# Kernel optimization log

Hardware: AMD Instinct MI355X
Metric: run time of the kernel (lower is better)

## Reference

```python
import jax, jax.numpy as jnp
import numpy as np

CHANNELS = 25
BN_EPS = 1e-5


def _diff(x):
    # x: [B,H,W]; zero-pad by 1 on H and W, then shifted slices (same as torch diff())
    xp = jnp.pad(x, ((0, 0), (1, 1), (1, 1)))
    p_x = (xp[:, 2:, 1:-1] - xp[:, :-2, 1:-1]) / 2
    p_y = (xp[:, 1:-1, 2:] - xp[:, 1:-1, :-2]) / 2
    pp_x = xp[:, 2:, 1:-1] + xp[:, :-2, 1:-1] - 2 * x
    pp_y = xp[:, 1:-1, 2:] + xp[:, 1:-1, :-2] - 2 * x
    pp_xy = xp[:, 2:, 2:] + xp[:, :-2, :-2] - xp[:, 2:, 1:-1] - xp[:, 1:-1, 2:]
    return p_x, p_y, pp_x, pp_y, pp_xy


def _batchnorm(x, gamma, beta):
    # x: [B,C,H,W]; training-mode BN with batch statistics (biased variance)
    mean = jnp.mean(x, axis=(0, 2, 3), keepdims=True)
    var = jnp.mean((x - mean) ** 2, axis=(0, 2, 3), keepdims=True)
    xhat = (x - mean) * jax.lax.rsqrt(var + BN_EPS)
    return xhat * gamma[None, :, None, None] + beta[None, :, None, None]


def setup_inputs() -> dict:
    key = jax.random.key(0)
    ks = jax.random.split(key, 5)
    B, H, W = 32, 512, 512
    x = jax.random.normal(ks[0], (B, H, W), dtype=jnp.float32)
    # 1x1 conv weights stored as [out_ch, in_ch]
    w1 = jax.random.normal(ks[1], (CHANNELS, 6), dtype=jnp.float32) * (1.0 / np.sqrt(6.0))
    b1 = jnp.zeros((CHANNELS,), dtype=jnp.float32)
    g1 = jnp.ones((CHANNELS,), dtype=jnp.float32)
    beta1 = jnp.zeros((CHANNELS,), dtype=jnp.float32)
    w2 = jax.random.normal(ks[2], (1, CHANNELS), dtype=jnp.float32) * (1.0 / np.sqrt(CHANNELS))
    b2 = jnp.zeros((1,), dtype=jnp.float32)
    g2 = jnp.ones((1,), dtype=jnp.float32)
    beta2 = jnp.zeros((1,), dtype=jnp.float32)
    return {"x": x, "w1": w1, "b1": b1, "g1": g1, "beta1": beta1,
            "w2": w2, "b2": b2, "g2": g2, "beta2": beta2}


def reference(x, w1, b1, g1, beta1, w2, b2, g2, beta2):
    p_x, p_y, pp_x, pp_y, pp_xy = _diff(x)
    xx = jnp.stack([x, p_x, p_y, pp_x, pp_y, pp_xy], axis=1)  # [B,6,H,W]
    # 1x1 conv == per-pixel channel matmul
    h = jnp.einsum('bchw,oc->bohw', xx, w1) + b1[None, :, None, None]
    h = jax.nn.relu(_batchnorm(h, g1, beta1))  # [B,25,H,W]
    o = jnp.einsum('bchw,oc->bohw', h, w2) + b2[None, :, None, None]
    o = jax.nn.relu(_batchnorm(o, g2, beta2))[:, 0, :, :]  # [B,H,W]
    return o + x
```

## Files before the change

kernel.cpp:

```cpp
#include <hip/hip_runtime.h>
#include <hip/hip_fp16.h>

typedef float f4 __attribute__((ext_vector_type(4)));
typedef float f2 __attribute__((ext_vector_type(2)));
typedef _Float16 f16x8 __attribute__((ext_vector_type(8)));
typedef float f32x16 __attribute__((ext_vector_type(16)));

#define NPIX (32*512*512)
#define BN_EPS 1e-5f


struct Rows { f4 C, N, S; float wv, ev, nwv, sev; };

__device__ __forceinline__ Rows loadrows(const float* __restrict__ x,
                                         const float* zbuf, int p) {
    Rows r;
    int rem = p & (512*512 - 1);
    int i = rem >> 9, jj = rem & 511;
    const float* xc = x + p;
    const float* xn = (i > 0)   ? xc - 512 : zbuf;
    const float* xs = (i < 511) ? xc + 512 : zbuf;
    r.C = *(const f4*)xc;
    r.N = *(const f4*)xn;
    r.S = *(const f4*)xs;
    bool hw = (jj > 0), he = (jj < 508);
    float wv  = xc[hw ? -1 : 0];
    float ev  = xc[he ?  4 : 3];
    float nwv = xn[hw ? -1 : 0];
    float sev = xs[he ?  4 : 3];
    r.wv  = hw ? wv  : 0.f;
    r.ev  = he ? ev  : 0.f;
    r.nwv = hw ? nwv : 0.f;
    r.sev = he ? sev : 0.f;
    return r;
}

__device__ __forceinline__ void mkstencil(const Rows& r, f4* s) {
    f4 E   = {r.C.y, r.C.z, r.C.w, r.ev};
    f4 W   = {r.wv,  r.C.x, r.C.y, r.C.z};
    f4 Ssh = {r.S.y, r.S.z, r.S.w, r.sev};
    f4 Nsh = {r.nwv, r.N.x, r.N.y, r.N.z};
    s[0] = r.C;
    s[1] = (r.S - r.N) * 0.5f;
    s[2] = (E - W) * 0.5f;
    s[3] = r.S + r.N - 2.f*r.C;
    s[4] = E + W - 2.f*r.C;
    s[5] = Ssh + Nsh - r.S - E;
}

__global__ __launch_bounds__(256) void k_moments(const float* __restrict__ x,
                                                 const float* __restrict__ ws,
                                                 float* __restrict__ outp) {
    const float* zbuf = ws + 496;
    int t = threadIdx.x;
    int g0 = blockIdx.x * 1024 + t;
    f2 acc[27];
    #pragma unroll
    for (int i = 0; i < 27; ++i) acc[i] = (f2){0.f, 0.f};

    #pragma unroll
    for (int q = 0; q < 4; ++q) {
        Rows r = loadrows(x, zbuf, (g0 + 256*q) * 4);
        f4 s[6];
        mkstencil(r, s);
        #pragma unroll
        for (int a = 0; a < 6; ++a) {
            f2 alo = s[a].xy, ahi = s[a].zw;
            asm("v_pk_add_f32 %0, %1, %0" : "+v"(acc[a]) : "v"(alo));
            asm("v_pk_add_f32 %0, %1, %0" : "+v"(acc[a]) : "v"(ahi));
            #pragma unroll
            for (int b = a; b < 6; ++b) {
                int idx = 6 + a*(11-a)/2 + b;
                f2 blo = s[b].xy, bhi = s[b].zw;
                asm("v_pk_fma_f32 %0, %1, %2, %0" : "+v"(acc[idx]) : "v"(alo), "v"(blo));
                asm("v_pk_fma_f32 %0, %1, %2, %0" : "+v"(acc[idx]) : "v"(ahi), "v"(bhi));
            }
        }
    }
    __shared__ float red[27][4];
    int wave = t >> 6, lane = t & 63;
    #pragma unroll
    for (int i = 0; i < 27; ++i) {
        float v = acc[i].x + acc[i].y;
        for (int off = 32; off; off >>= 1) v += __shfl_xor(v, off);
        if (lane == 0) red[i][wave] = v;
    }
    __syncthreads();
    if (t < 27)
        outp[t*2048 + blockIdx.x] = red[t][0] + red[t][1] + red[t][2] + red[t][3];
}

__global__ __launch_bounds__(256) void k_red(const float* __restrict__ outp,
                                             float* __restrict__ ws) {
    int b = blockIdx.x;
    int t = threadIdx.x;
    float v = 0.f;
    #pragma unroll
    for (int k = 0; k < 8; ++k) v += outp[b*2048 + t + 256*k];
    for (int off = 32; off; off >>= 1) v += __shfl_xor(v, off);
    __shared__ float red[4];
    int wave = t >> 6, lane = t & 63;
    if (lane == 0) red[wave] = v;
    __syncthreads();
    if (t == 0) ws[b] = red[0] + red[1] + red[2] + red[3];
}

__global__ void k_stats1(const float* w1, const float* b1, const float* g1,
                         const float* beta1, const float* w2, float* ws) {
    __shared__ float sm[32][8];
    int c = threadIdx.x;
    if (c < 32) {
        #pragma unroll
        for (int k = 0; k < 8; ++k) sm[c][k] = 0.f;
        ws[64 + c] = (c < 25) ? w2[c] : 0.f;
    }
    __syncthreads();
    if (c < 25) {
        const float invN = 1.f / (float)NPIX;
        float m1[6], wr[6];
        #pragma unroll
        for (int i = 0; i < 6; ++i) m1[i] = ws[i] * invN;
        #pragma unroll
        for (int i = 0; i < 6; ++i) wr[i] = w1[c*6 + i];
        float bc = b1[c];
        float mean = bc;
        #pragma unroll
        for (int i = 0; i < 6; ++i) mean = fmaf(wr[i], m1[i], mean);
        float e2 = bc * bc;
        #pragma unroll
        for (int i = 0; i < 6; ++i) e2 = fmaf(2.f*bc*wr[i], m1[i], e2);
        #pragma unroll
        for (int i = 0; i < 6; ++i)
            #pragma unroll
            for (int j = 0; j < 6; ++j) {
                int a = i < j ? i : j, b = i < j ? j : i;
                float m2 = ws[6 + a*(11-a)/2 + b] * invN;
                e2 = fmaf(wr[i]*wr[j], m2, e2);
            }
        float var = e2 - mean*mean;
        float a1 = g1[c] * rsqrtf(var + BN_EPS);
        #pragma unroll
        for (int i = 0; i < 6; ++i) sm[c][i] = a1 * wr[i];
        sm[c][6] = fmaf(a1, bc - mean, beta1[c]);
    }
    __syncthreads();
    int ch = c & 31, h = c >> 5;
    float aC=0.f, aN=0.f, aS=0.f, aE=0.f, aW=0.f, aNW=0.f, aSE=0.f, ab=0.f;
    if (h == 0) {
        float w0 = sm[ch][0], w1v = sm[ch][1], w2v = sm[ch][2];
        float w3 = sm[ch][3], w4v = sm[ch][4], w5 = sm[ch][5], be = sm[ch][6];
        aC  = w0 - 2.f*w3 - 2.f*w4v;
        aN  = -0.5f*w1v + w3;
        aS  =  0.5f*w1v + w3 - w5;
        aE  =  0.5f*w2v + w4v - w5;
        aW  = -0.5f*w2v + w4v;
        aNW = w5;
        aSE = w5;
        ab  = be;
    }
    __half2 p0 = __floats2half2_rn(aC,  aN);
    __half2 p1 = __floats2half2_rn(aS,  aE);
    __half2 p2 = __floats2half2_rn(aW,  aNW);
    __half2 p3 = __floats2half2_rn(aSE, ab);
    unsigned u0, u1, u2, u3;
    __builtin_memcpy(&u0, &p0, 4);
    __builtin_memcpy(&u1, &p1, 4);
    __builtin_memcpy(&u2, &p2, 4);
    __builtin_memcpy(&u3, &p3, 4);
    uint4 fr = {u0, u1, u2, u3};
    ((uint4*)(ws + 96))[c] = fr;
}

__global__ __launch_bounds__(256) void k_main(const float* __restrict__ x,
                                              const float* __restrict__ ws,
                                              const float* __restrict__ b2,
                                              float* __restrict__ stats,
                                              float* __restrict__ opre) {
    int t = threadIdx.x;
    int l = t & 63, wv = t >> 6;
    int lane31 = l & 31, h = l >> 5;
    const float* zb = ws + 1024;

    f16x8 afr;
    {
        uint4 u = ((const uint4*)(ws + 96))[l];
        union { uint4 u; f16x8 v; } cv; cv.u = u; afr = cv.v;
    }
    float w2v[16];
    #pragma unroll
    for (int r = 0; r < 16; ++r) {
        int creg = (r & 3) + 8 * (r >> 2);
        w2v[r] = ws[64 + creg + 4*h];
    }
    f32x16 zacc;
    #pragma unroll
    for (int r = 0; r < 16; ++r) zacc[r] = 0.f;
    float b2v = b2[0];
    float S1 = 0.f, S2 = 0.f;

    int wave_id = blockIdx.x * 4 + wv;
    #pragma unroll 1
    for (int rr = 0; rr < 2; ++rr) {
        int row = wave_id * 2 + rr;
        int i = row & 511;
        const float* xc = x + row * 512 + lane31;
        const float* xn = (i > 0)   ? xc - 512 : zb + lane31;
        const float* xs = (i < 511) ? xc + 512 : zb + lane31;
        float* op = opre + row * 512 + lane31;

        #pragma unroll
        for (int jt = 0; jt < 16; ++jt) {
            const int o4 = jt * 32;
            int offm1 = o4 - 1, offp1 = o4 + 1;
            if (jt == 0  && lane31 == 0)  offm1 = o4;
            if (jt == 15 && lane31 == 31) offp1 = o4;

            float C  = xc[o4];
            float W_ = xc[offm1];
            float E  = xc[offp1];
            float N  = xn[o4];
            float NW = xn[offm1];
            float S_ = xs[o4];
            float SE = xs[offp1];
            if (jt == 0)  { bool ok = (lane31 != 0);  W_ = ok ? W_ : 0.f; NW = ok ? NW : 0.f; }
            if (jt == 15) { bool ok = (lane31 != 31); E  = ok ? E  : 0.f; SE = ok ? SE : 0.f; }

            __half2 p0 = __floats2half2_rn(C,  N);
            __half2 p1 = __floats2half2_rn(S_, E);
            __half2 p2 = __floats2half2_rn(W_, NW);
            __half2 p3 = __floats2half2_rn(SE, 1.f);
            unsigned u0, u1, u2, u3;
            __builtin_memcpy(&u0, &p0, 4);
            __builtin_memcpy(&u1, &p1, 4);
            __builtin_memcpy(&u2, &p2, 4);
            __builtin_memcpy(&u3, &p3, 4);
            union { uint4 u; f16x8 v; } bv;
            bv.u = (uint4){u0, u1, u2, u3};

            f32x16 acc = __builtin_amdgcn_mfma_f32_32x32x16_f16(afr, bv.v, zacc, 0, 0, 0);

            float o = 0.f;
            #pragma unroll
            for (int r = 0; r < 16; ++r)
                o = fmaf(fmaxf(acc[r], 0.f), w2v[r], o);
            o += __shfl_xor(o, 32);
            o += b2v;
            S1 += o;
            S2 = fmaf(o, o, S2);
            if (l < 32) op[o4] = o;
        }
    }

    for (int off = 32; off; off >>= 1) { S1 += __shfl_xor(S1, off); S2 += __shfl_xor(S2, off); }
    __shared__ float red[2][4];
    if (l == 0) { red[0][wv] = S1; red[1][wv] = S2; }
    __syncthreads();
    if (t == 0) stats[2048 + blockIdx.x] = 0.5f*(red[0][0]+red[0][1]+red[0][2]+red[0][3]);
    if (t == 1) stats[4096 + blockIdx.x] = 0.5f*(red[1][0]+red[1][1]+red[1][2]+red[1][3]);
}

__global__ __launch_bounds__(256) void k_redS(float* __restrict__ ws) {
    int t = threadIdx.x;
    float s1 = 0.f, s2 = 0.f;
    #pragma unroll
    for (int k = 0; k < 8; ++k) {
        s1 += ws[2048 + t + 256*k];
        s2 += ws[4096 + t + 256*k];
    }
    for (int off = 32; off; off >>= 1) { s1 += __shfl_xor(s1, off); s2 += __shfl_xor(s2, off); }
    __shared__ float red[2][4];
    int wave = t >> 6, lane = t & 63;
    if (lane == 0) { red[0][wave] = s1; red[1][wave] = s2; }
    __syncthreads();
    if (t == 0) ws[27] = red[0][0] + red[0][1] + red[0][2] + red[0][3];
    if (t == 1) ws[28] = red[1][0] + red[1][1] + red[1][2] + red[1][3];
}

__global__ __launch_bounds__(256) void k_final(const float* __restrict__ x,
                                               const float* __restrict__ ws,
                                               const float* __restrict__ g2,
                                               const float* __restrict__ beta2,
                                               float* __restrict__ out) {
    const float invN = 1.f / (float)NPIX;
    float mean = ws[27] * invN;
    float var  = ws[28] * invN - mean*mean;
    float a2 = g2[0] * rsqrtf(var + BN_EPS);
    float c2 = fmaf(-mean, a2, beta2[0]);

    int idx = blockIdx.x * 256 + threadIdx.x;
    f4 o  = ((const f4*)out)[idx];
    f4 xv = ((const f4*)x)[idx];
    f4 r;
    r.x = fmaxf(fmaf(a2, o.x, c2), 0.f) + xv.x;
    r.y = fmaxf(fmaf(a2, o.y, c2), 0.f) + xv.y;
    r.z = fmaxf(fmaf(a2, o.z, c2), 0.f) + xv.z;
    r.w = fmaxf(fmaf(a2, o.w, c2), 0.f) + xv.w;
    ((f4*)out)[idx] = r;
}

extern "C" void kernel_launch(void* const* d_in, const int* in_sizes, int n_in,
                              void* d_out, int out_size, void* d_ws, size_t ws_size,
                              hipStream_t stream) {
    const float* x     = (const float*)d_in[0];
    const float* w1    = (const float*)d_in[1];
    const float* b1    = (const float*)d_in[2];
    const float* g1    = (const float*)d_in[3];
    const float* beta1 = (const float*)d_in[4];
    const float* w2    = (const float*)d_in[5];
    const float* b2    = (const float*)d_in[6];
    const float* g2    = (const float*)d_in[7];
    const float* beta2 = (const float*)d_in[8];
    float* out = (float*)d_out;
    float* ws  = (float*)d_ws;

    hipMemsetAsync(ws, 0, 8192, stream);
    k_moments<<<2048, 256, 0, stream>>>(x, ws, out);
    k_red    <<<27, 256, 0, stream>>>(out, ws);
    k_stats1 <<<1, 64, 0, stream>>>(w1, b1, g1, beta1, w2, ws);
    k_main   <<<2048, 256, 0, stream>>>(x, ws, b2, ws, out);
    k_redS   <<<1, 256, 0, stream>>>(ws);
    k_final  <<<8192, 256, 0, stream>>>(x, ws, g2, beta2, out);
}
```

Before: 100.2 us.

## Compute stencil second moments with MFMA Gram matrix and pack epilogue FMAs

The moments kernel now builds the six stencil features per pixel, stores them as fp16 in LDS along with a constant-one row, and accumulates the 7x7 Gram matrix with 32x32x16 MFMA instructions. This replaces the per-thread packed FMA outer products. It also changes the mapping to one wave per two rows with scalar loads. Separately, the main kernel's ReLU and w2 dot product are switched to packed v_pk_fma_f32 with paired weights. The trade-off is that fp16 moments lose precision, and there is extra LDS traffic and wave barriers per 64 pixels.

New measurement: 102.1 us. About the same (+1.9%).

```diff
diff --git a/kernel.cpp b/kernel.cpp
--- a/kernel.cpp
+++ b/kernel.cpp
@@ -10,84 +10,97 @@
 #define BN_EPS 1e-5f
 
 
-struct Rows { f4 C, N, S; float wv, ev, nwv, sev; };
-
-__device__ __forceinline__ Rows loadrows(const float* __restrict__ x,
-                                         const float* zbuf, int p) {
-    Rows r;
-    int rem = p & (512*512 - 1);
-    int i = rem >> 9, jj = rem & 511;
-    const float* xc = x + p;
-    const float* xn = (i > 0)   ? xc - 512 : zbuf;
-    const float* xs = (i < 511) ? xc + 512 : zbuf;
-    r.C = *(const f4*)xc;
-    r.N = *(const f4*)xn;
-    r.S = *(const f4*)xs;
-    bool hw = (jj > 0), he = (jj < 508);
-    float wv  = xc[hw ? -1 : 0];
-    float ev  = xc[he ?  4 : 3];
-    float nwv = xn[hw ? -1 : 0];
-    float sev = xs[he ?  4 : 3];
-    r.wv  = hw ? wv  : 0.f;
-    r.ev  = he ? ev  : 0.f;
-    r.nwv = hw ? nwv : 0.f;
-    r.sev = he ? sev : 0.f;
-    return r;
-}
-
-__device__ __forceinline__ void mkstencil(const Rows& r, f4* s) {
-    f4 E   = {r.C.y, r.C.z, r.C.w, r.ev};
-    f4 W   = {r.wv,  r.C.x, r.C.y, r.C.z};
-    f4 Ssh = {r.S.y, r.S.z, r.S.w, r.sev};
-    f4 Nsh = {r.nwv, r.N.x, r.N.y, r.N.z};
-    s[0] = r.C;
-    s[1] = (r.S - r.N) * 0.5f;
-    s[2] = (E - W) * 0.5f;
-    s[3] = r.S + r.N - 2.f*r.C;
-    s[4] = E + W - 2.f*r.C;
-    s[5] = Ssh + Nsh - r.S - E;
-}
-
 __global__ __launch_bounds__(256) void k_moments(const float* __restrict__ x,
                                                  const float* __restrict__ ws,
                                                  float* __restrict__ outp) {
-    const float* zbuf = ws + 496;
+    __shared__ ushort sl[4][8][64];
+    __shared__ float mom[4][7][7];
     int t = threadIdx.x;
-    int g0 = blockIdx.x * 1024 + t;
-    f2 acc[27];
-    #pragma unroll
-    for (int i = 0; i < 27; ++i) acc[i] = (f2){0.f, 0.f};
-
-    #pragma unroll
-    for (int q = 0; q < 4; ++q) {
-        Rows r = loadrows(x, zbuf, (g0 + 256*q) * 4);
-        f4 s[6];
-        mkstencil(r, s);
-        #pragma unroll
-        for (int a = 0; a < 6; ++a) {
-            f2 alo = s[a].xy, ahi = s[a].zw;
-            asm("v_pk_add_f32 %0, %1, %0" : "+v"(acc[a]) : "v"(alo));
-            asm("v_pk_add_f32 %0, %1, %0" : "+v"(acc[a]) : "v"(ahi));
-            #pragma unroll
-            for (int b = a; b < 6; ++b) {
-                int idx = 6 + a*(11-a)/2 + b;
-                f2 blo = s[b].xy, bhi = s[b].zw;
-                asm("v_pk_fma_f32 %0, %1, %2, %0" : "+v"(acc[idx]) : "v"(alo), "v"(blo));
-                asm("v_pk_fma_f32 %0, %1, %2, %0" : "+v"(acc[idx]) : "v"(ahi), "v"(bhi));
-            }
+    int l = t & 63, wv = t >> 6;
+    int h = l >> 5;
+    const float* zb = ws + 1024;
+
+    sl[wv][6][l] = (ushort)0x3C00;
+    sl[wv][7][l] = (ushort)0;
+
+    f32x16 accA, accB;
+    #pragma unroll
+    for (int r = 0; r < 16; ++r) { accA[r] = 0.f; accB[r] = 0.f; }
+
+    int arow = ((l & 31) < 7) ? (l & 31) : 7;
+    const ushort* rdp = &sl[wv][arow][8*h];
+
+    int wave_id = blockIdx.x * 4 + wv;
+    #pragma unroll 1
+    for (int rr = 0; rr < 2; ++rr) {
+        int row = wave_id * 2 + rr;
+        int i = row & 511;
+        const float* xr = x + row * 512;
+        const float* xn = (i > 0)   ? xr - 512 : zb;
+        const float* xs = (i < 511) ? xr + 512 : zb;
+        #pragma unroll 1
+        for (int it = 0; it < 8; ++it) {
+            int col = it * 64 + l;
+            bool okw = (col > 0), oke = (col < 511);
+            int cm = okw ? col - 1 : 0;
+            int cp = oke ? col + 1 : 511;
+            float C  = xr[col], N = xn[col], S_ = xs[col];
+            float W_ = xr[cm],  E = xr[cp];
+            float NW = xn[cm],  SE = xs[cp];
+            W_ = okw ? W_ : 0.f; NW = okw ? NW : 0.f;
+            E  = oke ? E  : 0.f; SE = oke ? SE : 0.f;
+
+            float s0 = C;
+            float s1 = (S_ - N) * 0.5f;
+            float s2 = (E - W_) * 0.5f;
+            float s3 = S_ + N - 2.f*C;
+            float s4 = E + W_ - 2.f*C;
+            float s5 = SE + NW - S_ - E;
+
+            __half h0 = __float2half(s0), h1 = __float2half(s1);
+            __half h2 = __float2half(s2), h3 = __float2half(s3);
+            __half h4 = __float2half(s4), h5 = __float2half(s5);
+            sl[wv][0][l] = *(ushort*)&h0;
+            sl[wv][1][l] = *(ushort*)&h1;
+            sl[wv][2][l] = *(ushort*)&h2;
+            sl[wv][3][l] = *(ushort*)&h3;
+            sl[wv][4][l] = *(ushort*)&h4;
+            sl[wv][5][l] = *(ushort*)&h5;
+            __builtin_amdgcn_wave_barrier();
+
+            union { uint4 u; f16x8 v; } f0, f1, f2_, f3;
+            f0.u  = *(const uint4*)(rdp);
+            f1.u  = *(const uint4*)(rdp + 16);
+            f2_.u = *(const uint4*)(rdp + 32);
+            f3.u  = *(const uint4*)(rdp + 48);
+            accA = __builtin_amdgcn_mfma_f32_32x32x16_f16(f0.v,  f0.v,  accA, 0, 0, 0);
+            accB = __builtin_amdgcn_mfma_f32_32x32x16_f16(f1.v,  f1.v,  accB, 0, 0, 0);
+            accA = __builtin_amdgcn_mfma_f32_32x32x16_f16(f2_.v, f2_.v, accA, 0, 0, 0);
+            accB = __builtin_amdgcn_mfma_f32_32x32x16_f16(f3.v,  f3.v,  accB, 0, 0, 0);
+            __builtin_amdgcn_wave_barrier();
         }
     }
-    __shared__ float red[27][4];
-    int wave = t >> 6, lane = t & 63;
-    #pragma unroll
-    for (int i = 0; i < 27; ++i) {
-        float v = acc[i].x + acc[i].y;
-        for (int off = 32; off; off >>= 1) v += __shfl_xor(v, off);
-        if (lane == 0) red[i][wave] = v;
-    }
-    __syncthreads();
-    if (t < 27)
-        outp[t*2048 + blockIdx.x] = red[t][0] + red[t][1] + red[t][2] + red[t][3];
+
+    if ((l & 31) < 7) {
+        int j = l & 31;
+        #pragma unroll
+        for (int r = 0; r < 4; ++r) {
+            int irow = r + 4*h;
+            if (irow < 7) mom[wv][irow][j] = accA[r] + accB[r];
+        }
+    }
+    __syncthreads();
+    if (t < 27) {
+        int a, b;
+        if (t < 6) { a = t; b = 6; }
+        else {
+            int rem = t - 6; a = 0;
+            while (rem >= 6 - a) { rem -= 6 - a; ++a; }
+            b = a + rem;
+        }
+        float v = mom[0][a][b] + mom[1][a][b] + mom[2][a][b] + mom[3][a][b];
+        outp[t*2048 + blockIdx.x] = v;
+    }
 }
 
 __global__ __launch_bounds__(256) void k_red(const float* __restrict__ outp,
@@ -186,11 +199,11 @@
         uint4 u = ((const uint4*)(ws + 96))[l];
         union { uint4 u; f16x8 v; } cv; cv.u = u; afr = cv.v;
     }
-    float w2v[16];
-    #pragma unroll
-    for (int r = 0; r < 16; ++r) {
-        int creg = (r & 3) + 8 * (r >> 2);
-        w2v[r] = ws[64 + creg + 4*h];
+    f2 w2p[8];
+    #pragma unroll
+    for (int r2 = 0; r2 < 8; ++r2) {
+        int creg = ((2*r2) & 3) + 8 * ((2*r2) >> 2) + 4*h;
+        w2p[r2] = *(const f2*)(ws + 64 + creg);
     }
     f32x16 zacc;
     #pragma unroll
@@ -239,10 +252,15 @@
 
             f32x16 acc = __builtin_amdgcn_mfma_f32_32x32x16_f16(afr, bv.v, zacc, 0, 0, 0);
 
-            float o = 0.f;
+            f2 oa = {0.f, 0.f};
             #pragma unroll
-            for (int r = 0; r < 16; ++r)
-                o = fmaf(fmaxf(acc[r], 0.f), w2v[r], o);
+            for (int r2 = 0; r2 < 8; ++r2) {
+                f2 rel;
+                rel.x = fmaxf(acc[2*r2],   0.f);
+                rel.y = fmaxf(acc[2*r2+1], 0.f);
+                asm("v_pk_fma_f32 %0, %1, %2, %0" : "+v"(oa) : "v"(rel), "v"(w2p[r2]));
+            }
+            float o = oa.x + oa.y;
             o += __shfl_xor(o, 32);
             o += b2v;
             S1 += o;
```
